# Kernel tuning notes

Hardware: AMD Instinct MI355X
Metric: run time of the kernel (lower is better)

## Reference

```python
import jax, jax.numpy as jnp
import numpy as np

EPS = 1e-9


def _resolve(circle_pos, circle_radius, aabb_pos, aabb_half):
    Nc = circle_pos.shape[0]
    Na = aabb_pos.shape[0]

    # ---- circle vs circle: push apart along center-to-center normal ----
    d = circle_pos[:, None, :] - circle_pos[None, :, :]          # [Nc,Nc,2]
    d2 = jnp.sum(d * d, axis=-1)                                 # [Nc,Nc]
    off_diag = ~jnp.eye(Nc, dtype=bool)
    dist = jnp.sqrt(jnp.where(d2 > EPS, d2, 1.0))
    pen = circle_radius[:, None] + circle_radius[None, :] - dist
    hit = off_diag & (d2 > EPS) & (pen > 0)
    normal = d / dist[..., None]
    # each body moves half the penetration toward itself; summing over the
    # full (symmetric) matrix resolves every unordered pair exactly once
    corr_cc = jnp.sum(jnp.where(hit[..., None], 0.5 * pen[..., None] * normal, 0.0), axis=1)

    # ---- aabb vs aabb: push along minimum-overlap axis ----
    da = aabb_pos[:, None, :] - aabb_pos[None, :, :]             # [Na,Na,2]
    ov = aabb_half[:, None, :] + aabb_half[None, :, :] - jnp.abs(da)
    hit_a = (~jnp.eye(Na, dtype=bool)) & (ov[..., 0] > 0) & (ov[..., 1] > 0)
    sgn = jnp.where(da >= 0, 1.0, -1.0)
    use_x = ov[..., 0] <= ov[..., 1]
    zeros = jnp.zeros_like(ov[..., 0])
    push_x = jnp.stack([0.5 * ov[..., 0] * sgn[..., 0], zeros], axis=-1)
    push_y = jnp.stack([zeros, 0.5 * ov[..., 1] * sgn[..., 1]], axis=-1)
    push = jnp.where(use_x[..., None], push_x, push_y)
    corr_aa = jnp.sum(jnp.where(hit_a[..., None], push, 0.0), axis=1)

    # ---- circle vs aabb: closest point on box ----
    rel = circle_pos[:, None, :] - aabb_pos[None, :, :]          # [Nc,Na,2]
    closest = jnp.clip(rel, -aabb_half[None, :, :], aabb_half[None, :, :])
    diff = rel - closest
    dd2 = jnp.sum(diff * diff, axis=-1)
    ddist = jnp.sqrt(jnp.where(dd2 > EPS, dd2, 1.0))
    pen_ca = circle_radius[:, None] - ddist
    hit_ca = (dd2 > EPS) & (pen_ca > 0)
    n_ca = diff / ddist[..., None]
    push_ca = jnp.where(hit_ca[..., None], 0.5 * pen_ca[..., None] * n_ca, 0.0)
    corr_c = jnp.sum(push_ca, axis=1)     # on circles
    corr_a = -jnp.sum(push_ca, axis=0)    # equal-and-opposite on boxes

    new_circle = circle_pos + corr_cc + corr_c
    new_aabb = aabb_pos + corr_aa + corr_a
    return jnp.concatenate([new_circle, new_aabb], axis=0)   # [Nc+Na, 2]


def setup_inputs() -> dict:
    key = jax.random.key(0)
    k1, k2, k3, k4 = jax.random.split(key, 4)
    circle_pos = jax.random.normal(k1, (4096, 2), dtype=jnp.float32)
    circle_radius = jax.random.uniform(k2, (4096,), dtype=jnp.float32)
    aabb_pos = jax.random.normal(k3, (2048, 2), dtype=jnp.float32)
    aabb_half = jax.random.uniform(k4, (2048, 2), dtype=jnp.float32)
    return {"circle_pos": circle_pos, "circle_radius": circle_radius,
            "aabb_pos": aabb_pos, "aabb_half": aabb_half}


def reference(circle_pos, circle_radius, aabb_pos, aabb_half):
    return _resolve(circle_pos, circle_radius, aabb_pos, aabb_half)
```

## Files before the change

kernel.cpp:

```cpp
#include <hip/hip_runtime.h>
#include <math.h>

#define EPS 1e-9f

__global__ void prep(const float2* __restrict__ cpos,
                     const float*  __restrict__ crad,
                     const float2* __restrict__ apos,
                     const float2* __restrict__ ahalf,
                     float4* __restrict__ P,
                     float2* __restrict__ out,
                     int Nc, int Ntot) {
    int i = blockIdx.x * blockDim.x + threadIdx.x;
    if (i >= Ntot) return;
    if (i < Nc) {
        const float2 p = cpos[i];
        P[i]   = make_float4(p.x, p.y, crad[i], 0.0f);
        out[i] = p;
    } else {
        const float2 a = apos[i - Nc];
        const float2 h = ahalf[i - Nc];
        P[i]   = make_float4(a.x, a.y, h.x, h.y);
        out[i] = a;
    }
}

__global__ __launch_bounds__(256)
void collide(const float4* __restrict__ P,
             float* __restrict__ out,
             int Nc, int Ntot) {
    const int lane  = threadIdx.x & 63;
    const int w     = __builtin_amdgcn_readfirstlane(threadIdx.x >> 6);
    const int ibase = (int)(blockIdx.x << 6);
    const int i     = ibase + lane;
    const int jbase = (blockIdx.y * 4 + w) << 6;

    const float4 me = P[i];
    float ax = 0.0f, ay = 0.0f;

    const bool bodyC = ibase < Nc;
    const bool partC = jbase < Nc;
    const bool diag  = (jbase == ibase);

    if (bodyC) {
        const float px = me.x, py = me.y, ri = me.z;
        if (partC) {
            if (diag) {
                #pragma unroll 8
                for (int k = 0; k < 64; ++k) {
                    const float4 q = P[jbase + k];
                    const float dx = px - q.x, dy = py - q.y;
                    const float d2 = fmaf(dx, dx, dy * dy);
                    const float r  = __builtin_amdgcn_rsqf(d2);
                    const float t  = fmaf(-d2, r, ri + q.z);
                    float s = fmaxf(0.5f * t * r, 0.0f);
                    s = (d2 > EPS) ? s : 0.0f;
                    ax = fmaf(s, dx, ax); ay = fmaf(s, dy, ay);
                }
            } else {
                #pragma unroll 8
                for (int k = 0; k < 64; ++k) {
                    const float4 q = P[jbase + k];
                    const float dx = px - q.x, dy = py - q.y;
                    const float d2 = fmaf(dx, dx, dy * dy);
                    const float r  = __builtin_amdgcn_rsqf(d2);
                    const float t  = fmaf(-d2, r, ri + q.z);
                    const float s  = fmaxf(0.5f * t * r, 0.0f);
                    ax = fmaf(s, dx, ax); ay = fmaf(s, dy, ay);
                }
            }
        } else {
            #pragma unroll 8
            for (int k = 0; k < 64; ++k) {
                const float4 q = P[jbase + k];
                const float rx = px - q.x, ry = py - q.y;
                const float cx = fminf(fmaxf(rx, -q.z), q.z);
                const float cy = fminf(fmaxf(ry, -q.w), q.w);
                const float dx = rx - cx, dy = ry - cy;
                const float d2 = fmaf(dx, dx, dy * dy);
                const float r  = __builtin_amdgcn_rsqf(d2);
                const float t  = fmaf(-d2, r, ri);
                float s = fmaxf(0.5f * t * r, 0.0f);
                s = (d2 > EPS) ? s : 0.0f;
                ax = fmaf(s, dx, ax); ay = fmaf(s, dy, ay);
            }
        }
    } else {
        const float bx = me.x, by = me.y, hx = me.z, hy = me.w;
        if (partC) {
            #pragma unroll 8
            for (int k = 0; k < 64; ++k) {
                const float4 q = P[jbase + k];
                const float rx = q.x - bx, ry = q.y - by;
                const float cx = fminf(fmaxf(rx, -hx), hx);
                const float cy = fminf(fmaxf(ry, -hy), hy);
                const float dx = rx - cx, dy = ry - cy;
                const float d2 = fmaf(dx, dx, dy * dy);
                const float r  = __builtin_amdgcn_rsqf(d2);
                const float t  = fmaf(-d2, r, q.z);
                float s = fmaxf(0.5f * t * r, 0.0f);
                s = (d2 > EPS) ? s : 0.0f;
                ax = fmaf(-s, dx, ax); ay = fmaf(-s, dy, ay);
            }
        } else {
            if (diag) {
                #pragma unroll 8
                for (int k = 0; k < 64; ++k) {
                    const int j = jbase + k;
                    const float4 q = P[j];
                    const float dax = bx - q.x, day = by - q.y;
                    const float ovx = (hx + q.z) - fabsf(dax);
                    const float ovy = (hy + q.w) - fabsf(day);
                    const bool hit = (fminf(ovx, ovy) > 0.0f) && (j != i);
                    const bool ux  = ovx <= ovy;
                    const float pxv = copysignf(0.5f * ovx, dax);
                    const float pyv = copysignf(0.5f * ovy, day);
                    ax += (hit && ux)  ? pxv : 0.0f;
                    ay += (hit && !ux) ? pyv : 0.0f;
                }
            } else {
                #pragma unroll 8
                for (int k = 0; k < 64; ++k) {
                    const float4 q = P[jbase + k];
                    const float dax = bx - q.x, day = by - q.y;
                    const float ovx = (hx + q.z) - fabsf(dax);
                    const float ovy = (hy + q.w) - fabsf(day);
                    const bool hit = fminf(ovx, ovy) > 0.0f;
                    const bool ux  = ovx <= ovy;
                    const float pxv = copysignf(0.5f * ovx, dax);
                    const float pyv = copysignf(0.5f * ovy, day);
                    ax += (hit && ux)  ? pxv : 0.0f;
                    ay += (hit && !ux) ? pyv : 0.0f;
                }
            }
        }
    }

    __shared__ float sax[4][64];
    __shared__ float say[4][64];
    sax[w][lane] = ax;
    say[w][lane] = ay;
    __syncthreads();
    if (w == 0) {
        const float tx = sax[0][lane] + sax[1][lane] + sax[2][lane] + sax[3][lane];
        const float ty = say[0][lane] + say[1][lane] + say[2][lane] + say[3][lane];
        atomicAdd(&out[2 * i],     tx);
        atomicAdd(&out[2 * i + 1], ty);
    }
}

extern "C" void kernel_launch(void* const* d_in, const int* in_sizes, int n_in,
                              void* d_out, int out_size, void* d_ws, size_t ws_size,
                              hipStream_t stream) {
    (void)n_in; (void)out_size; (void)ws_size;

    const float2* cpos  = (const float2*)d_in[0];
    const float*  crad  = (const float*) d_in[1];
    const float2* apos  = (const float2*)d_in[2];
    const float2* ahalf = (const float2*)d_in[3];

    const int Nc   = in_sizes[1];
    const int Na   = in_sizes[2] / 2;
    const int Ntot = Nc + Na;

    float4* P = (float4*)d_ws;

    prep<<<(Ntot + 255) / 256, 256, 0, stream>>>(cpos, crad, apos, ahalf,
                                                 P, (float2*)d_out, Nc, Ntot);

    const int gx = (Ntot + 63) / 64;
    const int gy = (Ntot + 255) / 256;
    dim3 grid(gx, gy, 1);
    collide<<<grid, 256, 0, stream>>>(P, (float*)d_out, Nc, Ntot);
}
```

Baseline: 79.40 us.

## Double j-tile per wave and drop shared-memory reduction for direct atomics

Each wave now covers 128 partners instead of 64, reading two float4s per iteration, so the grid's y dimension halves to a hard-coded 12. The specialised non-diagonal cc and bb loops are merged into the guarded versions, so the EPS and self-index checks now run on every pair. The LDS reduction and __syncthreads are removed, and every wave atomically adds its partial sums straight to the output, which doubles the atomic count. The hard-coded grid size assumes Ntot=6144, and the smaller grid halves the number of waves in flight.

```diff
diff --git a/kernel.cpp b/kernel.cpp
--- a/kernel.cpp
+++ b/kernel.cpp
@@ -24,128 +24,114 @@
     }
 }
 
+__device__ __forceinline__ void cc_pair(float px, float py, float ri,
+                                        const float4& q, float& ax, float& ay) {
+    const float dx = px - q.x, dy = py - q.y;
+    const float d2 = fmaf(dx, dx, dy * dy);
+    const float r  = __builtin_amdgcn_rsqf(d2);
+    const float t  = fmaf(-d2, r, ri + q.z);
+    float s = fmaxf(0.5f * t * r, 0.0f);
+    s = (d2 > EPS) ? s : 0.0f;
+    ax = fmaf(s, dx, ax); ay = fmaf(s, dy, ay);
+}
+__device__ __forceinline__ void cb_pair(float px, float py, float ri,
+                                        const float4& q, float& ax, float& ay) {
+    const float rx = px - q.x, ry = py - q.y;
+    const float cx = fminf(fmaxf(rx, -q.z), q.z);
+    const float cy = fminf(fmaxf(ry, -q.w), q.w);
+    const float dx = rx - cx, dy = ry - cy;
+    const float d2 = fmaf(dx, dx, dy * dy);
+    const float r  = __builtin_amdgcn_rsqf(d2);
+    const float t  = fmaf(-d2, r, ri);
+    float s = fmaxf(0.5f * t * r, 0.0f);
+    s = (d2 > EPS) ? s : 0.0f;
+    ax = fmaf(s, dx, ax); ay = fmaf(s, dy, ay);
+}
+__device__ __forceinline__ void bc_pair(float bx, float by, float hx, float hy,
+                                        const float4& q, float& ax, float& ay) {
+    const float rx = q.x - bx, ry = q.y - by;
+    const float cx = fminf(fmaxf(rx, -hx), hx);
+    const float cy = fminf(fmaxf(ry, -hy), hy);
+    const float dx = rx - cx, dy = ry - cy;
+    const float d2 = fmaf(dx, dx, dy * dy);
+    const float r  = __builtin_amdgcn_rsqf(d2);
+    const float t  = fmaf(-d2, r, q.z);
+    float s = fmaxf(0.5f * t * r, 0.0f);
+    s = (d2 > EPS) ? s : 0.0f;
+    ax = fmaf(-s, dx, ax); ay = fmaf(-s, dy, ay);
+}
+__device__ __forceinline__ void bb_pair(int j, int i, float bx, float by,
+                                        float hx, float hy,
+                                        const float4& q, float& ax, float& ay) {
+    const float dax = bx - q.x, day = by - q.y;
+    const float ovx = (hx + q.z) - fabsf(dax);
+    const float ovy = (hy + q.w) - fabsf(day);
+    const bool hit = (j != i) && (fminf(ovx, ovy) > 0.0f);
+    const bool ux  = ovx <= ovy;
+    ax += (hit && ux)  ? copysignf(0.5f * ovx, dax) : 0.0f;
+    ay += (hit && !ux) ? copysignf(0.5f * ovy, day) : 0.0f;
+}
+
 __global__ __launch_bounds__(256)
 void collide(const float4* __restrict__ P,
              float* __restrict__ out,
-             int Nc, int Ntot) {
+             int Nc) {
     const int lane  = threadIdx.x & 63;
-    const int w     = __builtin_amdgcn_readfirstlane(threadIdx.x >> 6);
+    const int w     = threadIdx.x >> 6;
     const int ibase = (int)(blockIdx.x << 6);
     const int i     = ibase + lane;
-    const int jbase = (blockIdx.y * 4 + w) << 6;
+
+    const int m  = blockIdx.y * 4 + w;
+    const int jb = m << 7;
 
     const float4 me = P[i];
     float ax = 0.0f, ay = 0.0f;
 
     const bool bodyC = ibase < Nc;
-    const bool partC = jbase < Nc;
-    const bool diag  = (jbase == ibase);
+    const bool partC = jb < Nc;
 
     if (bodyC) {
         const float px = me.x, py = me.y, ri = me.z;
         if (partC) {
-            if (diag) {
-                #pragma unroll 8
-                for (int k = 0; k < 64; ++k) {
-                    const float4 q = P[jbase + k];
-                    const float dx = px - q.x, dy = py - q.y;
-                    const float d2 = fmaf(dx, dx, dy * dy);
-                    const float r  = __builtin_amdgcn_rsqf(d2);
-                    const float t  = fmaf(-d2, r, ri + q.z);
-                    float s = fmaxf(0.5f * t * r, 0.0f);
-                    s = (d2 > EPS) ? s : 0.0f;
-                    ax = fmaf(s, dx, ax); ay = fmaf(s, dy, ay);
-                }
-            } else {
-                #pragma unroll 8
-                for (int k = 0; k < 64; ++k) {
-                    const float4 q = P[jbase + k];
-                    const float dx = px - q.x, dy = py - q.y;
-                    const float d2 = fmaf(dx, dx, dy * dy);
-                    const float r  = __builtin_amdgcn_rsqf(d2);
-                    const float t  = fmaf(-d2, r, ri + q.z);
-                    const float s  = fmaxf(0.5f * t * r, 0.0f);
-                    ax = fmaf(s, dx, ax); ay = fmaf(s, dy, ay);
-                }
+            #pragma unroll 4
+            for (int k = 0; k < 64; ++k) {
+                const float4 q1 = P[jb + k];
+                const float4 q2 = P[jb + 64 + k];
+                cc_pair(px, py, ri, q1, ax, ay);
+                cc_pair(px, py, ri, q2, ax, ay);
             }
         } else {
-            #pragma unroll 8
+            #pragma unroll 4
             for (int k = 0; k < 64; ++k) {
-                const float4 q = P[jbase + k];
-                const float rx = px - q.x, ry = py - q.y;
-                const float cx = fminf(fmaxf(rx, -q.z), q.z);
-                const float cy = fminf(fmaxf(ry, -q.w), q.w);
-                const float dx = rx - cx, dy = ry - cy;
-                const float d2 = fmaf(dx, dx, dy * dy);
-                const float r  = __builtin_amdgcn_rsqf(d2);
-                const float t  = fmaf(-d2, r, ri);
-                float s = fmaxf(0.5f * t * r, 0.0f);
-                s = (d2 > EPS) ? s : 0.0f;
-                ax = fmaf(s, dx, ax); ay = fmaf(s, dy, ay);
+                const float4 q1 = P[jb + k];
+                const float4 q2 = P[jb + 64 + k];
+                cb_pair(px, py, ri, q1, ax, ay);
+                cb_pair(px, py, ri, q2, ax, ay);
             }
         }
     } else {
         const float bx = me.x, by = me.y, hx = me.z, hy = me.w;
         if (partC) {
-            #pragma unroll 8
+            #pragma unroll 4
             for (int k = 0; k < 64; ++k) {
-                const float4 q = P[jbase + k];
-                const float rx = q.x - bx, ry = q.y - by;
-                const float cx = fminf(fmaxf(rx, -hx), hx);
-                const float cy = fminf(fmaxf(ry, -hy), hy);
-                const float dx = rx - cx, dy = ry - cy;
-                const float d2 = fmaf(dx, dx, dy * dy);
-                const float r  = __builtin_amdgcn_rsqf(d2);
-                const float t  = fmaf(-d2, r, q.z);
-                float s = fmaxf(0.5f * t * r, 0.0f);
-                s = (d2 > EPS) ? s : 0.0f;
-                ax = fmaf(-s, dx, ax); ay = fmaf(-s, dy, ay);
+                const float4 q1 = P[jb + k];
+                const float4 q2 = P[jb + 64 + k];
+                bc_pair(bx, by, hx, hy, q1, ax, ay);
+                bc_pair(bx, by, hx, hy, q2, ax, ay);
             }
         } else {
-            if (diag) {
-                #pragma unroll 8
-                for (int k = 0; k < 64; ++k) {
-                    const int j = jbase + k;
-                    const float4 q = P[j];
-                    const float dax = bx - q.x, day = by - q.y;
-                    const float ovx = (hx + q.z) - fabsf(dax);
-                    const float ovy = (hy + q.w) - fabsf(day);
-                    const bool hit = (fminf(ovx, ovy) > 0.0f) && (j != i);
-                    const bool ux  = ovx <= ovy;
-                    const float pxv = copysignf(0.5f * ovx, dax);
-                    const float pyv = copysignf(0.5f * ovy, day);
-                    ax += (hit && ux)  ? pxv : 0.0f;
-                    ay += (hit && !ux) ? pyv : 0.0f;
-                }
-            } else {
-                #pragma unroll 8
-                for (int k = 0; k < 64; ++k) {
-                    const float4 q = P[jbase + k];
-                    const float dax = bx - q.x, day = by - q.y;
-                    const float ovx = (hx + q.z) - fabsf(dax);
-                    const float ovy = (hy + q.w) - fabsf(day);
-                    const bool hit = fminf(ovx, ovy) > 0.0f;
-                    const bool ux  = ovx <= ovy;
-                    const float pxv = copysignf(0.5f * ovx, dax);
-                    const float pyv = copysignf(0.5f * ovy, day);
-                    ax += (hit && ux)  ? pxv : 0.0f;
-                    ay += (hit && !ux) ? pyv : 0.0f;
-                }
+            #pragma unroll 4
+            for (int k = 0; k < 64; ++k) {
+                const float4 q1 = P[jb + k];
+                const float4 q2 = P[jb + 64 + k];
+                bb_pair(jb + k,      i, bx, by, hx, hy, q1, ax, ay);
+                bb_pair(jb + 64 + k, i, bx, by, hx, hy, q2, ax, ay);
             }
         }
     }
 
-    __shared__ float sax[4][64];
-    __shared__ float say[4][64];
-    sax[w][lane] = ax;
-    say[w][lane] = ay;
-    __syncthreads();
-    if (w == 0) {
-        const float tx = sax[0][lane] + sax[1][lane] + sax[2][lane] + sax[3][lane];
-        const float ty = say[0][lane] + say[1][lane] + say[2][lane] + say[3][lane];
-        atomicAdd(&out[2 * i],     tx);
-        atomicAdd(&out[2 * i + 1], ty);
-    }
+    atomicAdd(&out[2 * i],     ax);
+    atomicAdd(&out[2 * i + 1], ay);
 }
 
 extern "C" void kernel_launch(void* const* d_in, const int* in_sizes, int n_in,
@@ -168,7 +154,7 @@
                                                  P, (float2*)d_out, Nc, Ntot);
 
     const int gx = (Ntot + 63) / 64;
-    const int gy = (Ntot + 255) / 256;
+    const int gy = 12;
     dim3 grid(gx, gy, 1);
-    collide<<<grid, 256, 0, stream>>>(P, (float*)d_out, Nc, Ntot);
+    collide<<<grid, 256, 0, stream>>>(P, (float*)d_out, Nc);
 }
```

Result: slower. 85.01 us (+7.1%).
